# Performance work log

Measured on AMD Instinct MI355X. Metric: run time of the kernel, lower is better.

Reference implementation:

```python
import jax, jax.numpy as jnp
import numpy as np
from itertools import product

S, P = 48, 4  # states, stacks


def _gen_i(p):
    # multi-indices (i_top..., i_nonempty...) over {None,0,1,2,3}, top constrained to {None, nonempty}
    subs = (None, 0, 1, 2, 3)
    for i_ne in product(subs, repeat=p):
        cands = [(None,) if j is None else (None, j) for j in i_ne]
        for i_top in product(*cands):
            yield (*i_top, *i_ne)


def _build_cd(s, p):
    # ConfigurationDetector1 weights: (s*9^p, 8p+s) indicator matrix + bias
    rows, cols = s * 9 ** p, 8 * p + s
    w = np.zeros((rows, cols), np.float32)
    b = np.zeros(rows, np.float32)
    zcols = 8 * p + np.arange(s)
    c = 0
    for i in _gen_i(p):
        idx = [a + 4 * t for t, a in enumerate(i) if a is not None]
        k = len(idx)
        r = np.arange(c, c + s)
        if k == 0:
            w[r, zcols] = 1.0
        else:
            w[c:c + s, idx] = 1.0
            w[r, zcols] = k * (4 * p + 2)
            b[r] = -k * (4 * p + 2)
        c += s
    return w, b


def setup_inputs() -> dict:
    s, p = S, P
    B = 10 * p * p
    key = jax.random.key(0)
    k1, k2, k3 = jax.random.split(key, 3)

    w_cd, b_cd = _build_cd(s, p)

    W_stack = np.zeros((p, 4 * p), np.float32)  # sums groups of 4 (shared by linear_stack/linear_top)
    for k in range(p):
        W_stack[k, 4 * k:4 * k + 4] = 1.0

    W_nstack = np.zeros((4 * p, p), np.float32)
    b_nstack = np.zeros(4 * p, np.float32)
    for i in range(p):
        W_nstack[4 * i + 0, i] = 1.0
        W_nstack[4 * i + 1, i] = 1.0 / B; b_nstack[4 * i + 1] = (B - 4 * p - 1) / B
        W_nstack[4 * i + 2, i] = 1.0 / B; b_nstack[4 * i + 2] = (B - 1) / B
        W_nstack[4 * i + 3, i] = float(B); b_nstack[4 * i + 3] = -B + 4 * p + 1

    W_ntop = np.zeros((4 * p, p), np.float32)
    for i in range(p):
        W_ntop[4 * i + 3, i] = -4.0 * p

    W_subtop = (2 * p + 1) * B * np.eye(4 * p, dtype=np.float32)
    b_subtop = -(2 * p + 1) * (B - 2) * np.ones(4 * p, np.float32)
    W_subne = B * np.eye(4 * p, dtype=np.float32)
    b_subne = -(B - 4 * p - 2) * np.ones(4 * p, np.float32)

    n = s * 9 ** p
    W_beta = jax.random.normal(k1, (s, n), jnp.float32) / np.sqrt(n)
    W_gamma = jax.random.normal(k2, (4 * p, n), jnp.float32) / np.sqrt(n)
    x = jax.random.normal(k3, (s + 12 * p,), jnp.float32)

    return {
        'x': x,
        'W_cd': jnp.asarray(w_cd), 'b_cd': jnp.asarray(b_cd),
        'W_stack': jnp.asarray(W_stack),
        'W_beta': W_beta, 'W_gamma': W_gamma,
        'W_nstack': jnp.asarray(W_nstack), 'b_nstack': jnp.asarray(b_nstack),
        'W_ntop': jnp.asarray(W_ntop),
        'W_subtop': jnp.asarray(W_subtop), 'b_subtop': jnp.asarray(b_subtop),
        'W_subne': jnp.asarray(W_subne), 'b_subne': jnp.asarray(b_subne),
    }


def _sat(v):
    # saturated_relu: clamp to [0, 1]
    return jnp.clip(v, 0.0, 1.0)


def reference(x, W_cd, b_cd, W_stack, W_beta, W_gamma, W_nstack, b_nstack,
              W_ntop, W_subtop, b_subtop, W_subne, b_subne):
    s = W_beta.shape[0]
    p = W_stack.shape[0]
    state = x[:s]
    noisy_sub_stack = x[s:s + 4 * p]
    noisy_sub_top = x[s + 4 * p:s + 8 * p]
    noisy_sub_nonempty = x[s + 8 * p:]

    w_in = jnp.concatenate([noisy_sub_top, noisy_sub_nonempty, state])  # (8p+s,)
    cd_out = _sat(W_cd @ w_in + b_cd)  # (s*9^p,)

    stack = W_stack @ _sat(noisy_sub_stack)  # (p,)
    top = W_stack @ _sat(noisy_sub_top)      # (p,)

    next_state = W_beta @ cd_out  # (s,)
    next_noisy_sub_stack = (W_nstack @ stack + b_nstack) + (W_ntop @ top) + (W_gamma @ cd_out) - 1.0  # (4p,)
    next_noisy_sub_top = W_subtop @ next_noisy_sub_stack + b_subtop
    next_noisy_sub_nonempty = W_subne @ next_noisy_sub_stack + b_subne

    return jnp.concatenate([next_state, next_noisy_sub_stack,
                            next_noisy_sub_top, next_noisy_sub_nonempty])
```

## Files before the change

kernel.cpp:

```cpp
#include <hip/hip_runtime.h>


#define NIN 80
#define CHUNK 256

__device__ __forceinline__ float satf(float v) {
    return fminf(fmaxf(v, 0.f), 1.f);
}

__global__ __launch_bounds__(256) void ss_main(
    const float* __restrict__ x,
    const float* __restrict__ Wb,
    const float* __restrict__ Wg,
    float* __restrict__ partials,
    int N, int nchunk)
{
    __shared__ float win[NIN];
    __shared__ float cd[CHUNK];
    const int t = threadIdx.x;
    if (t < NIN) win[t] = (t < 32) ? x[64 + t] : x[t - 32];

    const int wv = t >> 6, lane = t & 63;
    const float* Wrow0 = (wv == 3) ? Wg : (Wb + (size_t)(16 * wv) * N);

    float acc[16];
    #pragma unroll
    for (int s = 0; s < 16; ++s) acc[s] = 0.f;

    for (int c = blockIdx.x; c < nchunk; c += gridDim.x) {
        const int base = c * CHUNK;
        __syncthreads();

        {
            const int idx = base + t;
            float v = 0.f;
            if (idx < N) {
                const int pat = idx / 48;
                const int jrow = idx - pat * 48;
                int rem = pat;
                int kf = 0;
                int e0 = 0, e1 = 0, e2 = 0, e3 = 0;
                {
                    const int cnt0 = 729 << kf;
                    if (rem >= cnt0) { rem -= cnt0; const int q = rem >> (kf + 1);
                        const int d = q / 729; rem -= d * (729 << (kf + 1)); e0 = d + 1; kf++; }
                }
                {
                    const int cnt0 = 81 << kf;
                    if (rem >= cnt0) { rem -= cnt0; const int q = rem >> (kf + 1);
                        const int d = q / 81; rem -= d * (81 << (kf + 1)); e1 = d + 1; kf++; }
                }
                {
                    const int cnt0 = 9 << kf;
                    if (rem >= cnt0) { rem -= cnt0; const int q = rem >> (kf + 1);
                        const int d = q / 9; rem -= d * (9 << (kf + 1)); e2 = d + 1; kf++; }
                }
                {
                    const int cnt0 = 1 << kf;
                    if (rem >= cnt0) { rem -= cnt0; const int q = rem >> (kf + 1);
                        const int d = q; rem -= d * (1 << (kf + 1)); e3 = d + 1; kf++; }
                }
                float S = 0.f;
                int k = 0, r = 0;
                if (e0 > 0) { const int j = e0 - 1; S += win[16 + j]; k++;
                    if ((rem >> (kf - 1 - r)) & 1) { S += win[j]; k++; } r++; }
                if (e1 > 0) { const int j = e1 - 1; S += win[20 + j]; k++;
                    if ((rem >> (kf - 1 - r)) & 1) { S += win[4 + j]; k++; } r++; }
                if (e2 > 0) { const int j = e2 - 1; S += win[24 + j]; k++;
                    if ((rem >> (kf - 1 - r)) & 1) { S += win[8 + j]; k++; } r++; }
                if (e3 > 0) { const int j = e3 - 1; S += win[28 + j]; k++;
                    if ((rem >> (kf - 1 - r)) & 1) { S += win[12 + j]; k++; } r++; }
                const float stv = win[32 + jrow];
                v = (k == 0) ? stv : (S + 18.f * (float)k * (stv - 1.f));
                v = satf(v);
            }
            cd[t] = v;
        }
        __syncthreads();

        const int pos = base + 4 * lane;
        if (pos < N) {
            const float4 c4 = *reinterpret_cast<const float4*>(&cd[4 * lane]);
            #pragma unroll
            for (int s = 0; s < 16; ++s) {
                const float4 w4 = *reinterpret_cast<const float4*>(
                    Wrow0 + (size_t)s * N + pos);
                acc[s] += w4.x * c4.x + w4.y * c4.y + w4.z * c4.z + w4.w * c4.w;
            }
        }
    }

    #pragma unroll
    for (int s = 0; s < 16; ++s) {
        float v = acc[s];
        v += __shfl_xor(v, 32); v += __shfl_xor(v, 16); v += __shfl_xor(v, 8);
        v += __shfl_xor(v, 4);  v += __shfl_xor(v, 2);  v += __shfl_xor(v, 1);
        acc[s] = v;
    }
    if (lane == 0) {
        const int G = gridDim.x;
        #pragma unroll
        for (int s = 0; s < 16; ++s)
            partials[(size_t)(16 * wv + s) * G + blockIdx.x] = acc[s];
    }
}

__global__ __launch_bounds__(256) void ss_reduce(
    const float* __restrict__ partials,
    float* __restrict__ red,
    int G)
{
    const int slot = blockIdx.x;
    const int t = threadIdx.x;
    const float* p = partials + (size_t)slot * G;
    float s = 0.f;
    for (int b = t; b < G; b += 256) s += p[b];
    s += __shfl_xor(s, 32); s += __shfl_xor(s, 16); s += __shfl_xor(s, 8);
    s += __shfl_xor(s, 4);  s += __shfl_xor(s, 2);  s += __shfl_xor(s, 1);
    __shared__ float w[4];
    if ((t & 63) == 0) w[t >> 6] = s;
    __syncthreads();
    if (t == 0) red[slot] = w[0] + w[1] + w[2] + w[3];
}

__global__ __launch_bounds__(64) void ss_tail(
    const float* __restrict__ x,
    const float* __restrict__ Wstack,
    const float* __restrict__ Wnstack,
    const float* __restrict__ bnstack,
    const float* __restrict__ Wntop,
    const float* __restrict__ Wsubtop,
    const float* __restrict__ bsubtop,
    const float* __restrict__ Wsubne,
    const float* __restrict__ bsubne,
    const float* __restrict__ red,
    float* __restrict__ out)
{
    __shared__ float gsum[16];
    __shared__ float nss[16];
    const int t = threadIdx.x;
    const float v0 = red[t];
    if (t < 48) out[t] = v0;
    else gsum[t - 48] = v0;
    __syncthreads();
    if (t < 16) {
        float stack[4], top[4];
        #pragma unroll
        for (int i = 0; i < 4; ++i) { stack[i] = 0.f; top[i] = 0.f; }
        #pragma unroll
        for (int jj = 0; jj < 16; ++jj) {
            const float ss = satf(x[48 + jj]);
            const float st = satf(x[64 + jj]);
            #pragma unroll
            for (int i = 0; i < 4; ++i) {
                stack[i] += Wstack[i * 16 + jj] * ss;
                top[i]   += Wstack[i * 16 + jj] * st;
            }
        }
        float v = bnstack[t] + gsum[t] - 1.f;
        #pragma unroll
        for (int i = 0; i < 4; ++i)
            v += Wnstack[t * 4 + i] * stack[i] + Wntop[t * 4 + i] * top[i];
        nss[t] = v;
    }
    __syncthreads();
    if (t < 16) {
        float a = bsubtop[t], b2 = bsubne[t];
        #pragma unroll
        for (int k = 0; k < 16; ++k) {
            a  += Wsubtop[t * 16 + k] * nss[k];
            b2 += Wsubne[t * 16 + k] * nss[k];
        }
        out[48 + t] = nss[t];
        out[64 + t] = a;
        out[80 + t] = b2;
    }
}

extern "C" void kernel_launch(void* const* d_in, const int* in_sizes, int n_in,
                              void* d_out, int out_size, void* d_ws, size_t ws_size,
                              hipStream_t stream) {
    const float* x    = (const float*)d_in[0];
    const float* Wstk = (const float*)d_in[3];
    const float* Wb   = (const float*)d_in[4];
    const float* Wg   = (const float*)d_in[5];
    const float* Wns  = (const float*)d_in[6];
    const float* bns  = (const float*)d_in[7];
    const float* Wnt  = (const float*)d_in[8];
    const float* Wst  = (const float*)d_in[9];
    const float* bst  = (const float*)d_in[10];
    const float* Wsn  = (const float*)d_in[11];
    const float* bsn  = (const float*)d_in[12];
    float* out = (float*)d_out;
    float* partials = (float*)d_ws;

    const int N = in_sizes[2];
    const int nchunk = (N + CHUNK - 1) / CHUNK;
    int G = nchunk;
    const size_t maxG = (ws_size / sizeof(float) - 64) / 64;
    if ((size_t)G > maxG) G = (int)maxG;
    float* red = partials + (size_t)64 * G;

    ss_main<<<G, 256, 0, stream>>>(x, Wb, Wg, partials, N, nchunk);
    ss_reduce<<<64, 256, 0, stream>>>(partials, red, G);
    ss_tail<<<1, 64, 0, stream>>>(x, Wstk, Wns, bns, Wnt, Wst, bst, Wsn, bsn,
                                  red, out);
}
```

Before: 30.08 us.

## Split configuration-detector computation into separate kernel before matvec

Splits the fused kernel into two launches. The first writes the saturated configuration-detector activations to workspace. The second loads all 16 weight float4s up front and reduces them against the stored activations, which removes the in-block syncthreads between decode and matvec and lets weight loads issue without waiting. The cost is an extra kernel launch plus a global round-trip of about 315K floats. It also drops the clamp that limited the grid to the workspace size, so it assumes the workspace is large enough.

```diff
diff --git a/kernel.cpp b/kernel.cpp
--- a/kernel.cpp
+++ b/kernel.cpp
@@ -8,100 +8,92 @@
     return fminf(fmaxf(v, 0.f), 1.f);
 }
 
-__global__ __launch_bounds__(256) void ss_main(
+__global__ __launch_bounds__(256) void ss_cd(
     const float* __restrict__ x,
+    float* __restrict__ cd,
+    int N)
+{
+    __shared__ float win[NIN];
+    const int t = threadIdx.x;
+    if (t < NIN) win[t] = (t < 32) ? x[64 + t] : x[t - 32];
+    __syncthreads();
+
+    const int idx = blockIdx.x * CHUNK + t;
+    if (idx >= N) return;
+    const int pat = (unsigned)idx / 48u;
+    const int jrow = idx - pat * 48;
+    int rem = pat;
+    int kf = 0;
+    int e0 = 0, e1 = 0, e2 = 0, e3 = 0;
+    {
+        const int cnt0 = 729 << kf;
+        if (rem >= cnt0) { rem -= cnt0; const int q = rem >> (kf + 1);
+            const int d = (unsigned)q / 729u; rem -= d * (729 << (kf + 1)); e0 = d + 1; kf++; }
+    }
+    {
+        const int cnt0 = 81 << kf;
+        if (rem >= cnt0) { rem -= cnt0; const int q = rem >> (kf + 1);
+            const int d = (unsigned)q / 81u; rem -= d * (81 << (kf + 1)); e1 = d + 1; kf++; }
+    }
+    {
+        const int cnt0 = 9 << kf;
+        if (rem >= cnt0) { rem -= cnt0; const int q = rem >> (kf + 1);
+            const int d = (unsigned)q / 9u; rem -= d * (9 << (kf + 1)); e2 = d + 1; kf++; }
+    }
+    {
+        const int cnt0 = 1 << kf;
+        if (rem >= cnt0) { rem -= cnt0; const int q = rem >> (kf + 1);
+            const int d = q; rem -= d * (1 << (kf + 1)); e3 = d + 1; kf++; }
+    }
+    float S = 0.f;
+    int k = 0, r = 0;
+    if (e0 > 0) { const int j = e0 - 1; S += win[16 + j]; k++;
+        if ((rem >> (kf - 1 - r)) & 1) { S += win[j]; k++; } r++; }
+    if (e1 > 0) { const int j = e1 - 1; S += win[20 + j]; k++;
+        if ((rem >> (kf - 1 - r)) & 1) { S += win[4 + j]; k++; } r++; }
+    if (e2 > 0) { const int j = e2 - 1; S += win[24 + j]; k++;
+        if ((rem >> (kf - 1 - r)) & 1) { S += win[8 + j]; k++; } r++; }
+    if (e3 > 0) { const int j = e3 - 1; S += win[28 + j]; k++;
+        if ((rem >> (kf - 1 - r)) & 1) { S += win[12 + j]; k++; } r++; }
+    const float stv = win[32 + jrow];
+    const float v = (k == 0) ? stv : fmaf(18.f * (float)k, stv - 1.f, S);
+    cd[idx] = satf(v);
+}
+
+__global__ __launch_bounds__(256) void ss_mv(
+    const float* __restrict__ cd,
     const float* __restrict__ Wb,
     const float* __restrict__ Wg,
     float* __restrict__ partials,
-    int N, int nchunk)
-{
-    __shared__ float win[NIN];
-    __shared__ float cd[CHUNK];
-    const int t = threadIdx.x;
-    if (t < NIN) win[t] = (t < 32) ? x[64 + t] : x[t - 32];
-
+    int N, int G)
+{
+    const int t = threadIdx.x;
     const int wv = t >> 6, lane = t & 63;
+    const int pos = blockIdx.x * CHUNK + 4 * lane;
     const float* Wrow0 = (wv == 3) ? Wg : (Wb + (size_t)(16 * wv) * N);
-
-    float acc[16];
+    const bool valid = pos < N;
+
+    float4 c4 = make_float4(0.f, 0.f, 0.f, 0.f);
+    float4 w[16];
+    if (valid) {
+        c4 = *reinterpret_cast<const float4*>(cd + pos);
+        #pragma unroll
+        for (int s2 = 0; s2 < 16; ++s2)
+            w[s2] = *reinterpret_cast<const float4*>(Wrow0 + (size_t)s2 * N + pos);
+    } else {
+        #pragma unroll
+        for (int s2 = 0; s2 < 16; ++s2)
+            w[s2] = make_float4(0.f, 0.f, 0.f, 0.f);
+    }
+
     #pragma unroll
-    for (int s = 0; s < 16; ++s) acc[s] = 0.f;
-
-    for (int c = blockIdx.x; c < nchunk; c += gridDim.x) {
-        const int base = c * CHUNK;
-        __syncthreads();
-
-        {
-            const int idx = base + t;
-            float v = 0.f;
-            if (idx < N) {
-                const int pat = idx / 48;
-                const int jrow = idx - pat * 48;
-                int rem = pat;
-                int kf = 0;
-                int e0 = 0, e1 = 0, e2 = 0, e3 = 0;
-                {
-                    const int cnt0 = 729 << kf;
-                    if (rem >= cnt0) { rem -= cnt0; const int q = rem >> (kf + 1);
-                        const int d = q / 729; rem -= d * (729 << (kf + 1)); e0 = d + 1; kf++; }
-                }
-                {
-                    const int cnt0 = 81 << kf;
-                    if (rem >= cnt0) { rem -= cnt0; const int q = rem >> (kf + 1);
-                        const int d = q / 81; rem -= d * (81 << (kf + 1)); e1 = d + 1; kf++; }
-                }
-                {
-                    const int cnt0 = 9 << kf;
-                    if (rem >= cnt0) { rem -= cnt0; const int q = rem >> (kf + 1);
-                        const int d = q / 9; rem -= d * (9 << (kf + 1)); e2 = d + 1; kf++; }
-                }
-                {
-                    const int cnt0 = 1 << kf;
-                    if (rem >= cnt0) { rem -= cnt0; const int q = rem >> (kf + 1);
-                        const int d = q; rem -= d * (1 << (kf + 1)); e3 = d + 1; kf++; }
-                }
-                float S = 0.f;
-                int k = 0, r = 0;
-                if (e0 > 0) { const int j = e0 - 1; S += win[16 + j]; k++;
-                    if ((rem >> (kf - 1 - r)) & 1) { S += win[j]; k++; } r++; }
-                if (e1 > 0) { const int j = e1 - 1; S += win[20 + j]; k++;
-                    if ((rem >> (kf - 1 - r)) & 1) { S += win[4 + j]; k++; } r++; }
-                if (e2 > 0) { const int j = e2 - 1; S += win[24 + j]; k++;
-                    if ((rem >> (kf - 1 - r)) & 1) { S += win[8 + j]; k++; } r++; }
-                if (e3 > 0) { const int j = e3 - 1; S += win[28 + j]; k++;
-                    if ((rem >> (kf - 1 - r)) & 1) { S += win[12 + j]; k++; } r++; }
-                const float stv = win[32 + jrow];
-                v = (k == 0) ? stv : (S + 18.f * (float)k * (stv - 1.f));
-                v = satf(v);
-            }
-            cd[t] = v;
-        }
-        __syncthreads();
-
-        const int pos = base + 4 * lane;
-        if (pos < N) {
-            const float4 c4 = *reinterpret_cast<const float4*>(&cd[4 * lane]);
-            #pragma unroll
-            for (int s = 0; s < 16; ++s) {
-                const float4 w4 = *reinterpret_cast<const float4*>(
-                    Wrow0 + (size_t)s * N + pos);
-                acc[s] += w4.x * c4.x + w4.y * c4.y + w4.z * c4.z + w4.w * c4.w;
-            }
-        }
-    }
-
-    #pragma unroll
-    for (int s = 0; s < 16; ++s) {
-        float v = acc[s];
+    for (int s2 = 0; s2 < 16; ++s2) {
+        float v = w[s2].x * c4.x + w[s2].y * c4.y
+                + w[s2].z * c4.z + w[s2].w * c4.w;
         v += __shfl_xor(v, 32); v += __shfl_xor(v, 16); v += __shfl_xor(v, 8);
         v += __shfl_xor(v, 4);  v += __shfl_xor(v, 2);  v += __shfl_xor(v, 1);
-        acc[s] = v;
-    }
-    if (lane == 0) {
-        const int G = gridDim.x;
-        #pragma unroll
-        for (int s = 0; s < 16; ++s)
-            partials[(size_t)(16 * wv + s) * G + blockIdx.x] = acc[s];
+        if (lane == 0)
+            partials[(size_t)(16 * wv + s2) * G + blockIdx.x] = v;
     }
 }
 
@@ -192,16 +184,16 @@
     const float* Wsn  = (const float*)d_in[11];
     const float* bsn  = (const float*)d_in[12];
     float* out = (float*)d_out;
-    float* partials = (float*)d_ws;
 
     const int N = in_sizes[2];
-    const int nchunk = (N + CHUNK - 1) / CHUNK;
-    int G = nchunk;
-    const size_t maxG = (ws_size / sizeof(float) - 64) / 64;
-    if ((size_t)G > maxG) G = (int)maxG;
-    float* red = partials + (size_t)64 * G;
-
-    ss_main<<<G, 256, 0, stream>>>(x, Wb, Wg, partials, N, nchunk);
+    const int G = (N + CHUNK - 1) / CHUNK;
+
+    float* cd       = (float*)d_ws;
+    float* partials = cd + N;
+    float* red      = partials + (size_t)64 * G;
+
+    ss_cd<<<G, 256, 0, stream>>>(x, cd, N);
+    ss_mv<<<G, 256, 0, stream>>>(cd, Wb, Wg, partials, N, G);
     ss_reduce<<<64, 256, 0, stream>>>(partials, red, G);
     ss_tail<<<1, 64, 0, stream>>>(x, Wstk, Wns, bns, Wnt, Wst, bst, Wsn, bsn,
                                   red, out);
```

Result: slower. 32.50 us (+8.0%).
